# Optimization experiments

Hardware: AMD Instinct MI355X
Metric: run time of the kernel (lower is better)

The kernel has to match this reference:

```python
import jax, jax.numpy as jnp
import numpy as np

ROLE_BITS = 20
NHEAD = 16
D_MODEL = 1024
D_KEY = D_MODEL // NHEAD  # 64
D_FIL = 512
DFF = 4096
EPS = 1e-5


def _ln(x, g, b):
    mu = jnp.mean(x, axis=-1, keepdims=True)
    var = jnp.mean(jnp.square(x - mu), axis=-1, keepdims=True)
    return (x - mu) * jax.lax.rsqrt(var + EPS) * g + b


def setup_inputs() -> dict:
    key = jax.random.key(0)
    ks = jax.random.split(key, 10)
    N, BSZ, MEM = 16384, 16, 8
    D_IN = D_FIL + ROLE_BITS  # 532
    values = jax.random.normal(ks[0], (N, D_FIL), jnp.float32)
    role_index = jax.random.randint(ks[1], (N,), 1, 2 ** ROLE_BITS)
    # every (batch, memory_slot) pair occupied -> static shapes (compression is a no-op)
    slot = jax.random.permutation(ks[2], jnp.tile(jnp.arange(BSZ * MEM), N // (BSZ * MEM)))
    batch_index = (slot // MEM).astype(jnp.int32)
    memory_index = (slot % MEM).astype(jnp.int32)
    query_vectors = jax.random.normal(ks[3], (NHEAD, D_KEY), jnp.float32) * (1.0 / np.sqrt(D_KEY))
    s = 0.02
    Wk = jax.random.normal(ks[4], (D_MODEL, D_IN), jnp.float32) * s
    Wv = jax.random.normal(ks[5], (D_MODEL, D_IN), jnp.float32) * s
    Wo = jax.random.normal(ks[6], (D_MODEL, D_MODEL), jnp.float32) * s
    W1 = jax.random.normal(ks[7], (DFF, D_MODEL), jnp.float32) * s
    W2 = jax.random.normal(ks[8], (D_MODEL, DFF), jnp.float32) * s
    return dict(
        values=values, role_index=role_index, batch_index=batch_index,
        memory_index=memory_index, query_vectors=query_vectors,
        Wk=Wk, Wv=Wv, Wo=Wo, bo=jnp.zeros((D_MODEL,), jnp.float32),
        W1=W1, b1=jnp.zeros((DFF,), jnp.float32),
        W2=W2, b2=jnp.zeros((D_MODEL,), jnp.float32),
        g_fil=jnp.ones((D_FIL,), jnp.float32), b_fil=jnp.zeros((D_FIL,), jnp.float32),
        g_mha=jnp.ones((D_IN,), jnp.float32), b_mha=jnp.zeros((D_IN,), jnp.float32),
        g_ff=jnp.ones((D_MODEL,), jnp.float32), b_ff=jnp.zeros((D_MODEL,), jnp.float32),
        g_out=jnp.ones((D_MODEL,), jnp.float32), b_out=jnp.zeros((D_MODEL,), jnp.float32),
        bsz=BSZ, memory_slots=MEM,
    )


def _tree_positional_encodings(role_index):
    # bit-expand role indices: column j is bit j of the role index
    bits = (jnp.bitwise_and(role_index[:, None], 2 ** jnp.arange(ROLE_BITS)) != 0).astype(jnp.float32)
    # locate the highest set bit (torch: flip + argmax)
    mi = jnp.argmax(bits[:, ::-1], axis=1)
    cm = ROLE_BITS - 1 - mi  # index of highest set bit
    bits = bits * (1.0 - jax.nn.one_hot(cm, ROLE_BITS, dtype=bits.dtype))  # zero it out
    branch = jnp.arange(ROLE_BITS)[None, :] < cm[:, None]
    return jnp.where(branch, (bits - 0.5) * 2.0, bits)  # {0,1} -> {-1,1} below MSB


def reference(values, role_index, batch_index, memory_index, query_vectors,
              Wk, Wv, Wo, bo, W1, b1, W2, b2,
              g_fil, b_fil, g_mha, b_mha, g_ff, b_ff, g_out, b_out,
              bsz, memory_slots):
    N = values.shape[0]
    T = bsz * memory_slots  # num_trees (all (batch, slot) pairs occupied)

    tpd = _tree_positional_encodings(role_index)
    x = jnp.concatenate([_ln(values, g_fil, b_fil), tpd], axis=1)  # [N, d_input]
    x = _ln(x, g_mha, b_mha)
    k = (x @ Wk.T).reshape(N, NHEAD, D_KEY)
    v = (x @ Wv.T).reshape(N, NHEAD, D_KEY)
    qkm = jnp.einsum('nhd,hd->nh', k, query_vectors)  # [N, H]

    # combined batch+memory mask: node n attends to flat tree t = b*mem + m
    node_slot = batch_index * memory_slots + memory_index  # [N]
    mask = node_slot[:, None] == jnp.arange(T)[None, :]  # [N, T]
    scores = jnp.where(mask[:, :, None], qkm[:, None, :], -1e9) / np.sqrt(D_KEY)
    attn = jax.nn.softmax(scores, axis=0)  # softmax over nodes, [N, T, H]
    out = jnp.einsum('nhv,nth->thv', v, attn).reshape(T, D_MODEL)

    # post-attention: proj_o + residual with flattened queries, LN, FF, LN
    r1 = (out @ Wo.T + bo) + query_vectors.reshape(-1)
    l1 = _ln(r1, g_ff, b_ff)
    ff = jax.nn.gelu(l1 @ W1.T + b1, approximate=False) @ W2.T + b2
    l2 = _ln(ff + r1, g_out, b_out)

    rectangle_out = l2.reshape(bsz, memory_slots, D_MODEL)
    agent_pad_mask = jnp.zeros((bsz, memory_slots), dtype=bool)
    return rectangle_out, agent_pad_mask
```

## Files before the change

### kernel.cpp

```cpp
#include <hip/hip_runtime.h>
#include <hip/hip_bf16.h>

typedef __hip_bfloat16 bf16;

#define N_NODES 16384
#define D_FIL 512
#define D_IN 532
#define D_MODEL 1024
#define NHEAD 16
#define D_KEY 64
#define DFF 4096
#define NTREE 128
#define MEM_SLOTS 8
#define NODES_PER_TREE 128
#define EPS 1e-5f
#define XSE 544
#define XSU 272
#define CSTR 32

__device__ inline float gelu_exact(float x) {
    return 0.5f * x * (1.0f + erff(x * 0.7071067811865476f));
}

__device__ inline void blockReduceSum2(float& a, float& b, float* sm) {
    int tid = threadIdx.x;
    int lane = tid & 63, wid = tid >> 6;
#pragma unroll
    for (int off = 32; off > 0; off >>= 1) {
        a += __shfl_down(a, off, 64);
        b += __shfl_down(b, off, 64);
    }
    if (lane == 0) { sm[wid] = a; sm[4 + wid] = b; }
    __syncthreads();
    if (tid == 0) {
        sm[8] = sm[0] + sm[1] + sm[2] + sm[3];
        sm[9] = sm[4] + sm[5] + sm[6] + sm[7];
    }
    __syncthreads();
    a = sm[8]; b = sm[9];
}

__global__ __launch_bounds__(256) void prep_kernel(
        const float* __restrict__ values, const int* __restrict__ role,
        const int* __restrict__ bidx, const int* __restrict__ midx,
        const float* __restrict__ g_fil, const float* __restrict__ b_fil,
        const float* __restrict__ g_mha, const float* __restrict__ b_mha,
        bf16* __restrict__ xs, int* __restrict__ counts,
        const float* __restrict__ q, const float* __restrict__ Wk,
        unsigned* __restrict__ wqb,
        const float* __restrict__ Wv, float* __restrict__ wvt) {
    int b = blockIdx.x;
    int tid = threadIdx.x;

    if (b < 16) {
        int h = b;
        __shared__ float qs[64];
        if (tid < 64) qs[tid] = q[h * 64 + tid];
        __syncthreads();
        for (int p = tid; p < XSU; p += 256) {
            unsigned out = 0u;
            if (p < 266) {
                float a0 = 0.f, a1 = 0.f;
                int j0 = 2 * p;
#pragma unroll 8
                for (int d = 0; d < 64; ++d) {
                    const float* wr = Wk + (size_t)(h * 64 + d) * D_IN;
                    a0 += qs[d] * wr[j0];
                    a1 += qs[d] * wr[j0 + 1];
                }
                unsigned u0 = (unsigned)__bfloat16_as_ushort(__float2bfloat16(a0));
                unsigned u1 = (unsigned)__bfloat16_as_ushort(__float2bfloat16(a1));
                out = (u1 << 16) | u0;
            }
            wqb[h * XSU + p] = out;
        }
        return;
    }

    if (b < 560) {
        __shared__ float tile[32][33];
        int vb = b - 16;
        int c0 = (vb & 31) * 32, j0 = (vb >> 5) * 32;
        int tx = tid & 31, ty = tid >> 5;
#pragma unroll
        for (int r = 0; r < 4; ++r) {
            int cc = ty + r * 8;
            int j = j0 + tx;
            tile[cc][tx] = (j < D_IN) ? Wv[(size_t)(c0 + cc) * D_IN + j] : 0.f;
        }
        __syncthreads();
#pragma unroll
        for (int r = 0; r < 4; ++r) {
            int j = j0 + ty + r * 8;
            if (j < D_IN) wvt[(size_t)j * D_MODEL + c0 + tx] = tile[tx][ty + r * 8];
        }
        return;
    }

    int wave = tid >> 6;
    int l = tid & 63;
    int n = (b - 560) * 4 + wave;

    const float4* vp = (const float4*)(values + (size_t)n * D_FIL + l * 8);
    float4 v0 = vp[0], v1 = vp[1];

    int row = 0;
    if (l == 0) {
        int slot = bidx[n] * MEM_SLOTS + midx[n];
        int pos = atomicAdd(&counts[slot * CSTR], 1);
        row = slot * NODES_PER_TREE + pos;
    }

    float s = v0.x + v0.y + v0.z + v0.w + v1.x + v1.y + v1.z + v1.w;
    float ss = v0.x * v0.x + v0.y * v0.y + v0.z * v0.z + v0.w * v0.w
             + v1.x * v1.x + v1.y * v1.y + v1.z * v1.z + v1.w * v1.w;
#pragma unroll
    for (int m = 1; m < 64; m <<= 1) {
        s += __shfl_xor(s, m, 64);
        ss += __shfl_xor(ss, m, 64);
    }
    float mu = s * (1.f / D_FIL);
    float var = ss * (1.f / D_FIL) - mu * mu;
    float rs = rsqrtf(var + EPS);

    const float4* gf = (const float4*)(g_fil + l * 8);
    const float4* bf = (const float4*)(b_fil + l * 8);
    float4 gf0 = gf[0], gf1 = gf[1], bf0 = bf[0], bf1 = bf[1];
    float y[8];
    y[0] = (v0.x - mu) * rs * gf0.x + bf0.x;
    y[1] = (v0.y - mu) * rs * gf0.y + bf0.y;
    y[2] = (v0.z - mu) * rs * gf0.z + bf0.z;
    y[3] = (v0.w - mu) * rs * gf0.w + bf0.w;
    y[4] = (v1.x - mu) * rs * gf1.x + bf1.x;
    y[5] = (v1.y - mu) * rs * gf1.y + bf1.y;
    y[6] = (v1.z - mu) * rs * gf1.z + bf1.z;
    y[7] = (v1.w - mu) * rs * gf1.w + bf1.w;

    int r = role[n];
    int cm = 31 - __clz(r);
    float s_t = 2.f * (float)(__popc(r) - 1) - (float)cm;
    float ss_t = (float)cm;

    float s2 = y[0] + y[1] + y[2] + y[3] + y[4] + y[5] + y[6] + y[7];
    float ss2 = y[0] * y[0] + y[1] * y[1] + y[2] * y[2] + y[3] * y[3]
              + y[4] * y[4] + y[5] * y[5] + y[6] * y[6] + y[7] * y[7];
#pragma unroll
    for (int m = 1; m < 64; m <<= 1) {
        s2 += __shfl_xor(s2, m, 64);
        ss2 += __shfl_xor(ss2, m, 64);
    }
    s2 += s_t; ss2 += ss_t;
    float mu2 = s2 * (1.f / D_IN);
    float var2 = ss2 * (1.f / D_IN) - mu2 * mu2;
    float rs2 = rsqrtf(var2 + EPS);

    const float4* gm = (const float4*)(g_mha + l * 8);
    const float4* bm = (const float4*)(b_mha + l * 8);
    float4 gm0 = gm[0], gm1 = gm[1], bm0 = bm[0], bm1 = bm[1];
    float x[8];
    x[0] = (y[0] - mu2) * rs2 * gm0.x + bm0.x;
    x[1] = (y[1] - mu2) * rs2 * gm0.y + bm0.y;
    x[2] = (y[2] - mu2) * rs2 * gm0.z + bm0.z;
    x[3] = (y[3] - mu2) * rs2 * gm0.w + bm0.w;
    x[4] = (y[4] - mu2) * rs2 * gm1.x + bm1.x;
    x[5] = (y[5] - mu2) * rs2 * gm1.y + bm1.y;
    x[6] = (y[6] - mu2) * rs2 * gm1.z + bm1.z;
    x[7] = (y[7] - mu2) * rs2 * gm1.w + bm1.w;

    row = __shfl(row, 0, 64);

    {
        unsigned us[8];
#pragma unroll
        for (int k = 0; k < 8; ++k)
            us[k] = (unsigned)__bfloat16_as_ushort(__float2bfloat16(x[k]));
        uint4 pk = make_uint4((us[1] << 16) | us[0], (us[3] << 16) | us[2],
                              (us[5] << 16) | us[4], (us[7] << 16) | us[6]);
        *(uint4*)((char*)xs + (size_t)row * (XSE * 2) + 16 * l) = pk;
    }

    if (l < 20) {
        int bit = (r >> l) & 1;
        float tpd = (l < cm) ? (bit ? 1.f : -1.f) : 0.f;
        float x2 = (tpd - mu2) * rs2 * g_mha[512 + l] + b_mha[512 + l];
        xs[(size_t)row * XSE + 512 + l] = __float2bfloat16(x2);
    } else if (l < 26) {
        ((unsigned*)xs)[(size_t)row * XSU + 266 + (l - 20)] = 0u;
    }
}

__global__ __launch_bounds__(256) void qkm_kernel(const unsigned* __restrict__ xsu,
                                                  const unsigned* __restrict__ wqb,
                                                  float* __restrict__ qkmp) {
    __shared__ unsigned wshw[16 * 274];
    int tid = threadIdx.x;
#pragma unroll
    for (int hh = 0; hh < 16; ++hh) {
        wshw[hh * 274 + tid] = wqb[hh * XSU + tid];
        if (tid < 16) wshw[hh * 274 + 256 + tid] = wqb[hh * XSU + 256 + tid];
    }
    __syncthreads();

    int h = tid & 15, rp = tid >> 4;
    int r0 = blockIdx.x * 32;
    const uint2* xr0 = (const uint2*)(xsu + (size_t)(r0 + 2 * rp) * XSU);
    const uint2* xr1 = (const uint2*)(xsu + (size_t)(r0 + 2 * rp + 1) * XSU);
    const uint2* wr  = (const uint2*)(wshw + h * 274);
    float a0 = 0.f, a1 = 0.f;
#pragma unroll 8
    for (int j = 0; j < 136; ++j) {
        uint2 wu = wr[j];
        uint2 xa = xr0[j];
        uint2 xb = xr1[j];
        float w0 = __uint_as_float(wu.x << 16), w1 = __uint_as_float(wu.x & 0xffff0000u);
        float w2 = __uint_as_float(wu.y << 16), w3 = __uint_as_float(wu.y & 0xffff0000u);
        a0 += __uint_as_float(xa.x << 16) * w0 + __uint_as_float(xa.x & 0xffff0000u) * w1
            + __uint_as_float(xa.y << 16) * w2 + __uint_as_float(xa.y & 0xffff0000u) * w3;
        a1 += __uint_as_float(xb.x << 16) * w0 + __uint_as_float(xb.x & 0xffff0000u) * w1
            + __uint_as_float(xb.y << 16) * w2 + __uint_as_float(xb.y & 0xffff0000u) * w3;
    }
    qkmp[(size_t)(r0 + 2 * rp) * NHEAD + h] = a0;
    qkmp[(size_t)(r0 + 2 * rp + 1) * NHEAD + h] = a1;
}

__global__ void attn_fused_kernel(const float* __restrict__ qkmp, const unsigned* __restrict__ xsu,
                                  const float* __restrict__ wvt, float* __restrict__ attn_out) {
    int hg = blockIdx.x, t = blockIdx.y, tid = threadIdx.x;
    __shared__ __align__(16) float a4[NODES_PER_TREE * 4];
    __shared__ float zs[4][536];

    for (int l = tid; l < NODES_PER_TREE * 4; l += 256) {
        int i = l >> 2, hh = l & 3;
        a4[l] = qkmp[(size_t)t * NODES_PER_TREE * NHEAD + i * 16 + hg * 4 + hh] * 0.125f;
    }
    __syncthreads();

    int hh = tid >> 6, lane = tid & 63;
    {
        float s0 = a4[lane * 4 + hh], s1 = a4[(lane + 64) * 4 + hh];
        float m = fmaxf(s0, s1);
#pragma unroll
        for (int off = 32; off > 0; off >>= 1) m = fmaxf(m, __shfl_xor(m, off, 64));
        float e0 = expf(s0 - m), e1 = expf(s1 - m);
        float sum = e0 + e1;
#pragma unroll
        for (int off = 32; off > 0; off >>= 1) sum += __shfl_xor(sum, off, 64);
        float inv = 1.0f / sum;
        a4[lane * 4 + hh] = e0 * inv;
        a4[(lane + 64) * 4 + hh] = e1 * inv;
    }
    __syncthreads();

    {
        bool hasT = tid < 10;
        float az[4][2] = {};
        float at[4][2] = {};
        const unsigned* xt = xsu + (size_t)t * NODES_PER_TREE * XSU;
        for (int i0 = 0; i0 < NODES_PER_TREE; i0 += 8) {
            unsigned u[8], u2[8];
            float4 av[8];
#pragma unroll
            for (int k = 0; k < 8; ++k) u[k] = xt[(size_t)(i0 + k) * XSU + tid];
#pragma unroll
            for (int k = 0; k < 8; ++k) u2[k] = hasT ? xt[(size_t)(i0 + k) * XSU + 256 + tid] : 0u;
#pragma unroll
            for (int k = 0; k < 8; ++k) av[k] = *(const float4*)(a4 + (i0 + k) * 4);
#pragma unroll
            for (int k = 0; k < 8; ++k) {
                float x0 = __uint_as_float(u[k] << 16);
                float x1 = __uint_as_float(u[k] & 0xffff0000u);
                float x2 = __uint_as_float(u2[k] << 16);
                float x3 = __uint_as_float(u2[k] & 0xffff0000u);
                float4 a = av[k];
                az[0][0] += a.x * x0; az[0][1] += a.x * x1;
                az[1][0] += a.y * x0; az[1][1] += a.y * x1;
                az[2][0] += a.z * x0; az[2][1] += a.z * x1;
                az[3][0] += a.w * x0; az[3][1] += a.w * x1;
                at[0][0] += a.x * x2; at[0][1] += a.x * x3;
                at[1][0] += a.y * x2; at[1][1] += a.y * x3;
                at[2][0] += a.z * x2; at[2][1] += a.z * x3;
                at[3][0] += a.w * x2; at[3][1] += a.w * x3;
            }
        }
#pragma unroll
        for (int k = 0; k < 4; ++k) {
            *(float2*)(&zs[k][2 * tid]) = make_float2(az[k][0], az[k][1]);
            if (hasT) *(float2*)(&zs[k][512 + 2 * tid]) = make_float2(at[k][0], at[k][1]);
        }
    }
    __syncthreads();

    int c = hg * 256 + tid;
    const float* wp = wvt + c;
    float acc0 = 0.f, acc1 = 0.f;
    for (int j0 = 0; j0 < 528; j0 += 8) {
        float wv[8];
#pragma unroll
        for (int k = 0; k < 8; ++k) wv[k] = wp[(size_t)(j0 + k) * D_MODEL];
#pragma unroll
        for (int k = 0; k < 8; k += 2) {
            acc0 += zs[hh][j0 + k] * wv[k];
            acc1 += zs[hh][j0 + k + 1] * wv[k + 1];
        }
    }
    {
        float wv[4];
#pragma unroll
        for (int k = 0; k < 4; ++k) wv[k] = wp[(size_t)(528 + k) * D_MODEL];
#pragma unroll
        for (int k = 0; k < 4; k += 2) {
            acc0 += zs[hh][528 + k] * wv[k];
            acc1 += zs[hh][528 + k + 1] * wv[k + 1];
        }
    }
    attn_out[(size_t)t * D_MODEL + c] = acc0 + acc1;
}

__global__ void gemm_sk_kernel(const float* __restrict__ A, const float* __restrict__ B,
                               float* __restrict__ Cpart, int N, int K, int nsb) {
    __shared__ __align__(16) float As[32 * 132];
    __shared__ __align__(16) float Bs[32 * 68];
    int tid = threadIdx.x;
    int col0 = blockIdx.x * 64;
    int k0 = blockIdx.y * nsb * 32;
    float* C = Cpart + (size_t)blockIdx.y * 128 * N;

    int ty = tid >> 4, tx = tid & 15;
    int ar = tid >> 3, akk = (tid & 7) * 4;
    int br = tid >> 2, bkk = (tid & 3) * 8;

    float acc[8][4] = {};

    for (int s = 0; s < nsb; ++s) {
        int kb = k0 + s * 32;
#pragma unroll
        for (int p = 0; p < 4; ++p) {
            int row = ar + p * 32;
            float4 fa = *(const float4*)(A + (size_t)row * K + kb + akk);
            As[(akk + 0) * 132 + row] = fa.x;
            As[(akk + 1) * 132 + row] = fa.y;
            As[(akk + 2) * 132 + row] = fa.z;
            As[(akk + 3) * 132 + row] = fa.w;
        }
        {
            const float* bp = B + (size_t)(col0 + br) * K + kb + bkk;
            float4 f0 = *(const float4*)(bp);
            float4 f1 = *(const float4*)(bp + 4);
            Bs[(bkk + 0) * 68 + br] = f0.x; Bs[(bkk + 1) * 68 + br] = f0.y;
            Bs[(bkk + 2) * 68 + br] = f0.z; Bs[(bkk + 3) * 68 + br] = f0.w;
            Bs[(bkk + 4) * 68 + br] = f1.x; Bs[(bkk + 5) * 68 + br] = f1.y;
            Bs[(bkk + 6) * 68 + br] = f1.z; Bs[(bkk + 7) * 68 + br] = f1.w;
        }
        __syncthreads();
#pragma unroll
        for (int k = 0; k < 32; ++k) {
            float4 a0 = *(const float4*)(As + k * 132 + ty * 8);
            float4 a1 = *(const float4*)(As + k * 132 + ty * 8 + 4);
            float4 bv = *(const float4*)(Bs + k * 68 + tx * 4);
            acc[0][0] += a0.x * bv.x; acc[0][1] += a0.x * bv.y; acc[0][2] += a0.x * bv.z; acc[0][3] += a0.x * bv.w;
            acc[1][0] += a0.y * bv.x; acc[1][1] += a0.y * bv.y; acc[1][2] += a0.y * bv.z; acc[1][3] += a0.y * bv.w;
            acc[2][0] += a0.z * bv.x; acc[2][1] += a0.z * bv.y; acc[2][2] += a0.z * bv.z; acc[2][3] += a0.z * bv.w;
            acc[3][0] += a0.w * bv.x; acc[3][1] += a0.w * bv.y; acc[3][2] += a0.w * bv.z; acc[3][3] += a0.w * bv.w;
            acc[4][0] += a1.x * bv.x; acc[4][1] += a1.x * bv.y; acc[4][2] += a1.x * bv.z; acc[4][3] += a1.x * bv.w;
            acc[5][0] += a1.y * bv.x; acc[5][1] += a1.y * bv.y; acc[5][2] += a1.y * bv.z; acc[5][3] += a1.y * bv.w;
            acc[6][0] += a1.z * bv.x; acc[6][1] += a1.z * bv.y; acc[6][2] += a1.z * bv.z; acc[6][3] += a1.z * bv.w;
            acc[7][0] += a1.w * bv.x; acc[7][1] += a1.w * bv.y; acc[7][2] += a1.w * bv.z; acc[7][3] += a1.w * bv.w;
        }
        __syncthreads();
    }
#pragma unroll
    for (int r = 0; r < 8; ++r) {
        float4 v = make_float4(acc[r][0], acc[r][1], acc[r][2], acc[r][3]);
        *(float4*)(C + (size_t)(ty * 8 + r) * N + col0 + tx * 4) = v;
    }
}

__global__ void ln_r1_kernel(const float* __restrict__ po, const float* __restrict__ bo,
                             const float* __restrict__ qvec, const float* __restrict__ g,
                             const float* __restrict__ b, float* __restrict__ r1,
                             float* __restrict__ l1) {
    int t = blockIdx.x, tid = threadIdx.x;
    __shared__ float sm[16];
    float e[4];
#pragma unroll
    for (int c = 0; c < 4; ++c) {
        int j = c * 256 + tid;
        float v = bo[j] + qvec[j];
#pragma unroll
        for (int s = 0; s < 8; ++s)
            v += po[(size_t)s * NTREE * D_MODEL + (size_t)t * D_MODEL + j];
        e[c] = v;
        r1[(size_t)t * D_MODEL + j] = v;
    }
    float s = e[0] + e[1] + e[2] + e[3];
    float ss = e[0] * e[0] + e[1] * e[1] + e[2] * e[2] + e[3] * e[3];
    blockReduceSum2(s, ss, sm);
    float mu = s * (1.f / D_MODEL);
    float var = ss * (1.f / D_MODEL) - mu * mu;
    float rs = rsqrtf(var + EPS);
#pragma unroll
    for (int c = 0; c < 4; ++c) {
        int j = c * 256 + tid;
        l1[(size_t)t * D_MODEL + j] = (e[c] - mu) * rs * g[j] + b[j];
    }
}

__global__ void gelu_reduce_kernel(const float* __restrict__ p1, const float* __restrict__ b1,
                                   float* __restrict__ h1) {
    int idx4 = (blockIdx.x * 256 + threadIdx.x) * 4;
    int col = idx4 & (DFF - 1);
    float4 v = *(const float4*)(b1 + col);
#pragma unroll
    for (int s = 0; s < 8; ++s) {
        float4 p = *(const float4*)(p1 + (size_t)s * NTREE * DFF + idx4);
        v.x += p.x; v.y += p.y; v.z += p.z; v.w += p.w;
    }
    v.x = gelu_exact(v.x); v.y = gelu_exact(v.y);
    v.z = gelu_exact(v.z); v.w = gelu_exact(v.w);
    *(float4*)(h1 + idx4) = v;
}

__global__ void ln_out_kernel(const float* __restrict__ p2, const float* __restrict__ b2,
                              const float* __restrict__ r1, const float* __restrict__ g,
                              const float* __restrict__ b, float* __restrict__ out) {
    int t = blockIdx.x, tid = threadIdx.x;
    __shared__ float sm[16];
    float e[4];
#pragma unroll
    for (int c = 0; c < 4; ++c) {
        int j = c * 256 + tid;
        float v = b2[j] + r1[(size_t)t * D_MODEL + j];
#pragma unroll
        for (int s = 0; s < 16; ++s)
            v += p2[(size_t)s * NTREE * D_MODEL + (size_t)t * D_MODEL + j];
        e[c] = v;
    }
    float s = e[0] + e[1] + e[2] + e[3];
    float ss = e[0] * e[0] + e[1] * e[1] + e[2] * e[2] + e[3] * e[3];
    blockReduceSum2(s, ss, sm);
    float mu = s * (1.f / D_MODEL);
    float var = ss * (1.f / D_MODEL) - mu * mu;
    float rs = rsqrtf(var + EPS);
#pragma unroll
    for (int c = 0; c < 4; ++c) {
        int j = c * 256 + tid;
        out[(size_t)t * D_MODEL + j] = (e[c] - mu) * rs * g[j] + b[j];
    }
    if (t == 0 && tid < 128) out[(size_t)NTREE * D_MODEL + tid] = 0.f;
}

extern "C" void kernel_launch(void* const* d_in, const int* in_sizes, int n_in,
                              void* d_out, int out_size, void* d_ws, size_t ws_size,
                              hipStream_t stream) {
    const float* values = (const float*)d_in[0];
    const int* role     = (const int*)d_in[1];
    const int* bidx     = (const int*)d_in[2];
    const int* midx     = (const int*)d_in[3];
    const float* qvec   = (const float*)d_in[4];
    const float* Wk     = (const float*)d_in[5];
    const float* Wv     = (const float*)d_in[6];
    const float* Wo     = (const float*)d_in[7];
    const float* bo     = (const float*)d_in[8];
    const float* W1     = (const float*)d_in[9];
    const float* b1     = (const float*)d_in[10];
    const float* W2     = (const float*)d_in[11];
    const float* b2     = (const float*)d_in[12];
    const float* g_fil  = (const float*)d_in[13];
    const float* b_fil  = (const float*)d_in[14];
    const float* g_mha  = (const float*)d_in[15];
    const float* b_mha  = (const float*)d_in[16];
    const float* g_ff   = (const float*)d_in[17];
    const float* b_ff   = (const float*)d_in[18];
    const float* g_out  = (const float*)d_in[19];
    const float* b_out  = (const float*)d_in[20];

    char* w = (char*)d_ws;
    unsigned* wqb   = (unsigned*)(w + 0);
    float* qkmp     = (float*)(w + 18432);
    float* attn_out = (float*)(w + 1068032);
    float* r1       = (float*)(w + 1592320);
    float* l1       = (float*)(w + 2116608);
    float* h1       = (float*)(w + 2640896);
    int*   counts   = (int*)  (w + 2640896);
    float* wvt      = (float*)(w + 4738048);
    char*  big      = w + 6917120;
    bf16*  xs = (bf16*)big;
    float* po = (float*)big;
    float* p1 = (float*)(big + 4194304);
    float* p2 = (float*)big;

    float* out = (float*)d_out;

    hipMemsetAsync(counts, 0, 128 * CSTR * sizeof(int), stream);

    prep_kernel<<<4656, 256, 0, stream>>>(values, role, bidx, midx,
                                          g_fil, b_fil, g_mha, b_mha,
                                          xs, counts,
                                          qvec, Wk, wqb, Wv, wvt);

    qkm_kernel<<<N_NODES / 32, 256, 0, stream>>>((const unsigned*)xs, wqb, qkmp);

    attn_fused_kernel<<<dim3(4, NTREE), 256, 0, stream>>>(qkmp, (const unsigned*)xs, wvt, attn_out);

    gemm_sk_kernel<<<dim3(16, 8), 256, 0, stream>>>(attn_out, Wo, po, D_MODEL, D_MODEL, 4);

    ln_r1_kernel<<<NTREE, 256, 0, stream>>>(po, bo, qvec, g_ff, b_ff, r1, l1);

    gemm_sk_kernel<<<dim3(64, 8), 256, 0, stream>>>(l1, W1, p1, DFF, D_MODEL, 4);

    gelu_reduce_kernel<<<512, 256, 0, stream>>>(p1, b1, h1);

    gemm_sk_kernel<<<dim3(16, 16), 256, 0, stream>>>(h1, W2, p2, D_MODEL, DFF, 8);

    ln_out_kernel<<<NTREE, 256, 0, stream>>>(p2, b2, r1, g_out, b_out, out);
}
```

Measured before the change: 260.3 us.

## Replace FP32 split-K GEMMs with split-bf16 MFMA GEMMs

Swaps the scalar FP32 tiled split-K GEMM used for the Wo, W1 and W2 projections for an MFMA kernel. Each fp32 operand is split into bf16 high and low parts, and three bf16 16x16x32 MFMAs per tile approximate fp32 accuracy. A is read straight from global memory into registers, and only B is staged in LDS. The W1 GEMM also moves from 8 to 4 K-splits, and the gelu reduction is changed to match, which cuts partial-sum traffic. The cost is a small loss of accuracy from the three-term bf16 split and extra conversion instructions per tile.

```diff
diff --git a/kernel.cpp b/kernel.cpp
--- a/kernel.cpp
+++ b/kernel.cpp
@@ -17,6 +17,12 @@
 #define XSE 544
 #define XSU 272
 #define CSTR 32
+#define BSTR 40
+
+typedef float f32x4 __attribute__((ext_vector_type(4)));
+typedef short s16x8 __attribute__((ext_vector_type(8)));
+
+union PackU { uint4 u; s16x8 s; };
 
 __device__ inline float gelu_exact(float x) {
     return 0.5f * x * (1.0f + erff(x * 0.7071067811865476f));
@@ -316,62 +322,101 @@
     attn_out[(size_t)t * D_MODEL + c] = acc0 + acc1;
 }
 
-__global__ void gemm_sk_kernel(const float* __restrict__ A, const float* __restrict__ B,
-                               float* __restrict__ Cpart, int N, int K, int nsb) {
-    __shared__ __align__(16) float As[32 * 132];
-    __shared__ __align__(16) float Bs[32 * 68];
+__global__ __launch_bounds__(256) void gemm_mfma_sk(const float* __restrict__ A,
+                                                    const float* __restrict__ B,
+                                                    float* __restrict__ Cpart,
+                                                    int N, int K, int nsb) {
+    __shared__ __align__(16) unsigned short bhi[64 * BSTR];
+    __shared__ __align__(16) unsigned short blo[64 * BSTR];
     int tid = threadIdx.x;
     int col0 = blockIdx.x * 64;
     int k0 = blockIdx.y * nsb * 32;
     float* C = Cpart + (size_t)blockIdx.y * 128 * N;
 
-    int ty = tid >> 4, tx = tid & 15;
-    int ar = tid >> 3, akk = (tid & 7) * 4;
-    int br = tid >> 2, bkk = (tid & 3) * 8;
-
-    float acc[8][4] = {};
+    int w = tid >> 6, l = tid & 63;
+    int l15 = l & 15, l4 = l >> 4;
+    int scol = tid >> 2, sk8 = (tid & 3) * 8;
+
+    f32x4 acc[2][4];
+#pragma unroll
+    for (int rt = 0; rt < 2; ++rt)
+#pragma unroll
+        for (int ct = 0; ct < 4; ++ct) acc[rt][ct] = (f32x4){0.f, 0.f, 0.f, 0.f};
 
     for (int s = 0; s < nsb; ++s) {
         int kb = k0 + s * 32;
-#pragma unroll
-        for (int p = 0; p < 4; ++p) {
-            int row = ar + p * 32;
-            float4 fa = *(const float4*)(A + (size_t)row * K + kb + akk);
-            As[(akk + 0) * 132 + row] = fa.x;
-            As[(akk + 1) * 132 + row] = fa.y;
-            As[(akk + 2) * 132 + row] = fa.z;
-            As[(akk + 3) * 132 + row] = fa.w;
-        }
+
         {
-            const float* bp = B + (size_t)(col0 + br) * K + kb + bkk;
-            float4 f0 = *(const float4*)(bp);
+            const float* bp = B + (size_t)(col0 + scol) * K + kb + sk8;
+            float4 f0 = *(const float4*)bp;
             float4 f1 = *(const float4*)(bp + 4);
-            Bs[(bkk + 0) * 68 + br] = f0.x; Bs[(bkk + 1) * 68 + br] = f0.y;
-            Bs[(bkk + 2) * 68 + br] = f0.z; Bs[(bkk + 3) * 68 + br] = f0.w;
-            Bs[(bkk + 4) * 68 + br] = f1.x; Bs[(bkk + 5) * 68 + br] = f1.y;
-            Bs[(bkk + 6) * 68 + br] = f1.z; Bs[(bkk + 7) * 68 + br] = f1.w;
+            float fe[8] = {f0.x, f0.y, f0.z, f0.w, f1.x, f1.y, f1.z, f1.w};
+            unsigned hu[4], lu[4];
+#pragma unroll
+            for (int p = 0; p < 4; ++p) {
+                unsigned u0 = __float_as_uint(fe[2 * p]);
+                unsigned u1 = __float_as_uint(fe[2 * p + 1]);
+                unsigned h0 = u0 & 0xffff0000u, h1 = u1 & 0xffff0000u;
+                float d0 = fe[2 * p] - __uint_as_float(h0);
+                float d1 = fe[2 * p + 1] - __uint_as_float(h1);
+                hu[p] = h1 | (u0 >> 16);
+                lu[p] = (__float_as_uint(d1) & 0xffff0000u) | (__float_as_uint(d0) >> 16);
+            }
+            *(uint4*)(&bhi[scol * BSTR + sk8]) = make_uint4(hu[0], hu[1], hu[2], hu[3]);
+            *(uint4*)(&blo[scol * BSTR + sk8]) = make_uint4(lu[0], lu[1], lu[2], lu[3]);
         }
         __syncthreads();
-#pragma unroll
-        for (int k = 0; k < 32; ++k) {
-            float4 a0 = *(const float4*)(As + k * 132 + ty * 8);
-            float4 a1 = *(const float4*)(As + k * 132 + ty * 8 + 4);
-            float4 bv = *(const float4*)(Bs + k * 68 + tx * 4);
-            acc[0][0] += a0.x * bv.x; acc[0][1] += a0.x * bv.y; acc[0][2] += a0.x * bv.z; acc[0][3] += a0.x * bv.w;
-            acc[1][0] += a0.y * bv.x; acc[1][1] += a0.y * bv.y; acc[1][2] += a0.y * bv.z; acc[1][3] += a0.y * bv.w;
-            acc[2][0] += a0.z * bv.x; acc[2][1] += a0.z * bv.y; acc[2][2] += a0.z * bv.z; acc[2][3] += a0.z * bv.w;
-            acc[3][0] += a0.w * bv.x; acc[3][1] += a0.w * bv.y; acc[3][2] += a0.w * bv.z; acc[3][3] += a0.w * bv.w;
-            acc[4][0] += a1.x * bv.x; acc[4][1] += a1.x * bv.y; acc[4][2] += a1.x * bv.z; acc[4][3] += a1.x * bv.w;
-            acc[5][0] += a1.y * bv.x; acc[5][1] += a1.y * bv.y; acc[5][2] += a1.y * bv.z; acc[5][3] += a1.y * bv.w;
-            acc[6][0] += a1.z * bv.x; acc[6][1] += a1.z * bv.y; acc[6][2] += a1.z * bv.z; acc[6][3] += a1.z * bv.w;
-            acc[7][0] += a1.w * bv.x; acc[7][1] += a1.w * bv.y; acc[7][2] += a1.w * bv.z; acc[7][3] += a1.w * bv.w;
+
+        s16x8 ah[2], al[2];
+#pragma unroll
+        for (int rt = 0; rt < 2; ++rt) {
+            const float* ap = A + (size_t)(32 * w + 16 * rt + l15) * K + kb + l4 * 8;
+            float4 f0 = *(const float4*)ap;
+            float4 f1 = *(const float4*)(ap + 4);
+            float fe[8] = {f0.x, f0.y, f0.z, f0.w, f1.x, f1.y, f1.z, f1.w};
+            unsigned hu[4], lu[4];
+#pragma unroll
+            for (int p = 0; p < 4; ++p) {
+                unsigned u0 = __float_as_uint(fe[2 * p]);
+                unsigned u1 = __float_as_uint(fe[2 * p + 1]);
+                unsigned h0 = u0 & 0xffff0000u, h1 = u1 & 0xffff0000u;
+                float d0 = fe[2 * p] - __uint_as_float(h0);
+                float d1 = fe[2 * p + 1] - __uint_as_float(h1);
+                hu[p] = h1 | (u0 >> 16);
+                lu[p] = (__float_as_uint(d1) & 0xffff0000u) | (__float_as_uint(d0) >> 16);
+            }
+            PackU uh, ul;
+            uh.u = make_uint4(hu[0], hu[1], hu[2], hu[3]);
+            ul.u = make_uint4(lu[0], lu[1], lu[2], lu[3]);
+            ah[rt] = uh.s;
+            al[rt] = ul.s;
+        }
+
+#pragma unroll
+        for (int ct = 0; ct < 4; ++ct) {
+            PackU rbh, rbl;
+            rbh.u = *(const uint4*)(&bhi[(16 * ct + l15) * BSTR + l4 * 8]);
+            rbl.u = *(const uint4*)(&blo[(16 * ct + l15) * BSTR + l4 * 8]);
+#pragma unroll
+            for (int rt = 0; rt < 2; ++rt) {
+                acc[rt][ct] = __builtin_amdgcn_mfma_f32_16x16x32_bf16(ah[rt], rbh.s, acc[rt][ct], 0, 0, 0);
+                acc[rt][ct] = __builtin_amdgcn_mfma_f32_16x16x32_bf16(al[rt], rbh.s, acc[rt][ct], 0, 0, 0);
+                acc[rt][ct] = __builtin_amdgcn_mfma_f32_16x16x32_bf16(ah[rt], rbl.s, acc[rt][ct], 0, 0, 0);
+            }
         }
         __syncthreads();
     }
-#pragma unroll
-    for (int r = 0; r < 8; ++r) {
-        float4 v = make_float4(acc[r][0], acc[r][1], acc[r][2], acc[r][3]);
-        *(float4*)(C + (size_t)(ty * 8 + r) * N + col0 + tx * 4) = v;
+
+#pragma unroll
+    for (int rt = 0; rt < 2; ++rt) {
+        int row = 32 * w + 16 * rt + l4 * 4;
+#pragma unroll
+        for (int ct = 0; ct < 4; ++ct) {
+            int col = col0 + 16 * ct + l15;
+#pragma unroll
+            for (int r = 0; r < 4; ++r)
+                C[(size_t)(row + r) * N + col] = acc[rt][ct][r];
+        }
     }
 }
 
@@ -411,7 +456,7 @@
     int col = idx4 & (DFF - 1);
     float4 v = *(const float4*)(b1 + col);
 #pragma unroll
-    for (int s = 0; s < 8; ++s) {
+    for (int s = 0; s < 4; ++s) {
         float4 p = *(const float4*)(p1 + (size_t)s * NTREE * DFF + idx4);
         v.x += p.x; v.y += p.y; v.z += p.z; v.w += p.w;
     }
@@ -502,15 +547,15 @@
 
     attn_fused_kernel<<<dim3(4, NTREE), 256, 0, stream>>>(qkmp, (const unsigned*)xs, wvt, attn_out);
 
-    gemm_sk_kernel<<<dim3(16, 8), 256, 0, stream>>>(attn_out, Wo, po, D_MODEL, D_MODEL, 4);
+    gemm_mfma_sk<<<dim3(16, 8), 256, 0, stream>>>(attn_out, Wo, po, D_MODEL, D_MODEL, 4);
 
     ln_r1_kernel<<<NTREE, 256, 0, stream>>>(po, bo, qvec, g_ff, b_ff, r1, l1);
 
-    gemm_sk_kernel<<<dim3(64, 8), 256, 0, stream>>>(l1, W1, p1, DFF, D_MODEL, 4);
+    gemm_mfma_sk<<<dim3(64, 4), 256, 0, stream>>>(l1, W1, p1, DFF, D_MODEL, 8);
 
     gelu_reduce_kernel<<<512, 256, 0, stream>>>(p1, b1, h1);
 
-    gemm_sk_kernel<<<dim3(16, 16), 256, 0, stream>>>(h1, W2, p2, D_MODEL, DFF, 8);
+    gemm_mfma_sk<<<dim3(16, 16), 256, 0, stream>>>(h1, W2, p2, D_MODEL, DFF, 8);
 
     ln_out_kernel<<<NTREE, 256, 0, stream>>>(p2, b2, r1, g_out, b_out, out);
 }
```

Measured after the change: 243.4 us. 1.07x faster.
